# Optimization experiments

Hardware: AMD Instinct MI355X
Metric: run time of the kernel (lower is better)

Reference implementation:

```python
import jax, jax.numpy as jnp
import numpy as np

DIM = 512
HEADS = 8
DIM_HEAD = 64
INNER = HEADS * DIM_HEAD  # 512
HIDDEN = 512 * 4          # mlp_dim * expansion
EPS = 1e-5
SCALE = DIM_HEAD ** -0.5


def layernorm(x, w, b):
    mu = jnp.mean(x, axis=-1, keepdims=True)
    var = jnp.var(x, axis=-1, keepdims=True)
    return (x - mu) * jax.lax.rsqrt(var + EPS) * w + b


def setup_inputs() -> dict:
    key = jax.random.key(0)
    ks = jax.random.split(key, 12)
    B, P, N = 2, 8, 1024  # P must equal HEADS (axis-swap bug in original rearrange)
    s = lambda k, shape, fan: jax.random.normal(k, shape, jnp.float32) * (fan ** -0.5)
    return {
        "x": jax.random.normal(ks[0], (B, P, N, DIM), jnp.float32),
        "ln0_w": jnp.ones((DIM,), jnp.float32),
        "ln0_b": jnp.zeros((DIM,), jnp.float32),
        "ln1_w": jnp.ones((DIM,), jnp.float32),
        "ln1_b": jnp.zeros((DIM,), jnp.float32),
        "w_qkv": s(ks[1], (DIM, 3 * INNER), DIM),
        "w_o": s(ks[2], (INNER, DIM), INNER),
        "b_o": jnp.zeros((DIM,), jnp.float32),
        "w1": s(ks[3], (DIM, HIDDEN), DIM),
        "b1": jnp.zeros((HIDDEN,), jnp.float32),
        "w2": s(ks[4], (HIDDEN, DIM), HIDDEN),
        "b2": jnp.zeros((DIM,), jnp.float32),
    }


def reference(x, ln0_w, ln0_b, ln1_w, ln1_b, w_qkv, w_o, b_o, w1, b1, w2, b2):
    B, P, N, _ = x.shape
    x = layernorm(x, ln0_w, ln0_b)  # outer block norm

    # ---- VisionAttention ----
    h = layernorm(x, ln1_w, ln1_b)
    qkv = h @ w_qkv                                    # [B,P,N,3*INNER]
    q, k, v = jnp.split(qkv, 3, axis=-1)
    def to_heads(t):  # [B,P,N,H*D] -> [B,H,P,N,D]
        return t.reshape(B, P, N, HEADS, DIM_HEAD).transpose(0, 3, 1, 2, 4)
    q, k, v = to_heads(q), to_heads(k), to_heads(v)
    dots = jnp.einsum("bhpnd,bhpmd->bhpnm", q, k) * SCALE  # full NxN scores
    attn = jax.nn.softmax(dots, axis=-1)
    out = jnp.einsum("bhpnm,bhpmd->bhpnd", attn, v)        # [B,H,P,N,D]
    # Faithful to buggy rearrange 'b p h n d -> b p n (h d)': swaps H and P axes.
    out = out.transpose(0, 1, 3, 2, 4).reshape(B, HEADS, N, P * DIM_HEAD)
    out = out @ w_o + b_o                                  # [B,H,N,DIM]
    x = out + x  # residual (valid because P == HEADS)

    # ---- MLP ----
    m = jax.nn.gelu(x @ w1 + b1, approximate=False) @ w2 + b2
    return m + x
```

## Files before the change

### kernel.cpp

```cpp
#include <hip/hip_runtime.h>
#include <hip/hip_bf16.h>
#include <math.h>

#define DIMV 512
#define NTOK 16384
#define NSEQ 1024
#define HEADSV 8
#define PPV 8
#define DHEAD 64
#define QKVW 1536
#define HIDV 2048
#define SC2 0.18033688011112042f

typedef unsigned short ushort;
typedef unsigned int uint;
typedef __attribute__((ext_vector_type(8))) short short8;
typedef __attribute__((ext_vector_type(8))) unsigned short ushort8;
typedef __attribute__((ext_vector_type(4))) unsigned short ushortx4;
typedef __attribute__((ext_vector_type(4))) float floatx4;

__device__ __forceinline__ float bf2f(ushort u){
  union { unsigned int i; float f; } c; c.i = ((unsigned int)u) << 16; return c.f;
}
__device__ __forceinline__ ushort f2bf(float f){
  union { float f; unsigned int i; } c; c.f = f;
  unsigned int u = c.i + 0x7fffu + ((c.i >> 16) & 1u);
  return (ushort)(u >> 16);
}
__device__ __forceinline__ void async_copy16(const void* gptr, void* lptr){
  __builtin_amdgcn_global_load_lds((const __attribute__((address_space(1))) void*)gptr,
                                   (__attribute__((address_space(3))) void*)lptr, 16, 0, 0);
}
__device__ __forceinline__ float fast_gelu(float x){
  float u = x * (2.3022084f + 0.1029435f * x * x);
  return x * __builtin_amdgcn_rcpf(1.f + exp2f(-u));
}

__device__ __forceinline__ void wave_reduce2(float& a, float& b){
  #pragma unroll
  for (int off = 32; off > 0; off >>= 1){
    a += __shfl_down(a, off, 64);
    b += __shfl_down(b, off, 64);
  }
}

__device__ __forceinline__ void wtrans_body(const float* __restrict__ W,
    __hip_bfloat16* __restrict__ Wt, int K, int N, int bx, int by, int t,
    float* tile ){
  int bn = bx * 32, bk = by * 32;
  int tx = t & 31, ty = t >> 5;
  #pragma unroll
  for (int i = 0; i < 32; i += 8)
    tile[(ty + i) * 33 + tx] = W[(size_t)(bk + ty + i) * N + bn + tx];
  __syncthreads();
  #pragma unroll
  for (int i = 0; i < 32; i += 8)
    Wt[(size_t)(bn + ty + i) * K + bk + tx] = __float2bfloat16(tile[tx * 33 + ty + i]);
}

__global__ __launch_bounds__(256) void prep_kernel(const float* __restrict__ x,
    const float* __restrict__ w0, const float* __restrict__ b0,
    const float* __restrict__ w1ln, const float* __restrict__ b1ln,
    __hip_bfloat16* __restrict__ x1, __hip_bfloat16* __restrict__ h,
    const float* __restrict__ wqkv, __hip_bfloat16* __restrict__ wqkvT,
    const float* __restrict__ wo,   __hip_bfloat16* __restrict__ woT,
    const float* __restrict__ w1,   __hip_bfloat16* __restrict__ w1T,
    const float* __restrict__ w2,   __hip_bfloat16* __restrict__ w2T){
  __shared__ float smem[32 * 33];
  int bid = blockIdx.x;
  int t = threadIdx.x;
  if (bid >= NTOK){
    int r = bid - NTOK;
    if (r < 768)        wtrans_body(wqkv, wqkvT, 512, 1536, r % 48, r / 48, t, smem);
    else if (r < 1024){ r -= 768;  wtrans_body(wo, woT, 512, 512,  r % 16, r / 16, t, smem); }
    else if (r < 2048){ r -= 1024; wtrans_body(w1, w1T, 512, 2048, r % 64, r / 64, t, smem); }
    else             { r -= 2048; wtrans_body(w2, w2T, 2048, 512, r % 16, r / 16, t, smem); }
    return;
  }
  float* sm = smem;
  size_t row = bid;
  const float2* xr = (const float2*)(x + row * DIMV);
  float2 v = xr[t];
  float s = v.x + v.y;
  float sq = v.x * v.x + v.y * v.y;
  wave_reduce2(s, sq);
  int wid = t >> 6, lane = t & 63;
  if (lane == 0){ sm[wid] = s; sm[8 + wid] = sq; }
  __syncthreads();
  s  = sm[0] + sm[1] + sm[2] + sm[3];
  sq = sm[8] + sm[9] + sm[10] + sm[11];
  float mu = s * (1.f / DIMV);
  float var = sq * (1.f / DIMV) - mu * mu;
  float r = rsqrtf(var + 1e-5f);
  float2 ww = ((const float2*)w0)[t];
  float2 bb = ((const float2*)b0)[t];
  float2 y;
  y.x = (v.x - mu) * r * ww.x + bb.x;
  y.y = (v.y - mu) * r * ww.y + bb.y;
  ushort2 xb; xb.x = f2bf(y.x); xb.y = f2bf(y.y);
  ((ushort2*)(x1 + row * DIMV))[t] = xb;
  float s2 = y.x + y.y, sq2 = y.x * y.x + y.y * y.y;
  wave_reduce2(s2, sq2);
  __syncthreads();
  if (lane == 0){ sm[wid] = s2; sm[8 + wid] = sq2; }
  __syncthreads();
  s2  = sm[0] + sm[1] + sm[2] + sm[3];
  sq2 = sm[8] + sm[9] + sm[10] + sm[11];
  float mu2 = s2 * (1.f / DIMV);
  float var2 = sq2 * (1.f / DIMV) - mu2 * mu2;
  float r2 = rsqrtf(var2 + 1e-5f);
  float2 w1v = ((const float2*)w1ln)[t];
  float2 b1v = ((const float2*)b1ln)[t];
  float hx = (y.x - mu2) * r2 * w1v.x + b1v.x;
  float hy = (y.y - mu2) * r2 * w1v.y + b1v.y;
  ushort2 hb; hb.x = f2bf(hx); hb.y = f2bf(hy);
  ((ushort2*)(h + row * DIMV))[t] = hb;
}

template<int SWAP>
__global__ __launch_bounds__(512, 2) void gemm_8p(
    const __hip_bfloat16* __restrict__ A,
    const __hip_bfloat16* __restrict__ Bt,
    const float* __restrict__ bias,
    __hip_bfloat16* __restrict__ Cb,
    ushort* __restrict__ vt,
    int M, int N, int K, int gx, int dogelu)
{
  __shared__ __hip_bfloat16 As[2][256 * 64];
  __shared__ __hip_bfloat16 Bs[2][256 * 64];
  int tid = threadIdx.x;
  int l = tid & 63, w = tid >> 6;
  int wr = w >> 2, wc = w & 3;
  int fm = l & 15, quad = l >> 4;

  int bid = blockIdx.x;
  int xcd = bid & 7, idx = bid >> 3;
  int xl = idx % gx, yl = idx / gx;
  size_t bm = (size_t)(xcd * 8 + yl) * 256;
  size_t bn = (size_t)xl * 256;

  int sr = tid >> 3;
  int sc = ((tid & 7) ^ (sr & 7)) * 8;
  const __hip_bfloat16* Ab0 = A + (bm + sr) * (size_t)K + sc;
  const __hip_bfloat16* Bb0 = Bt + (bn + sr) * (size_t)K + sc;
  int ldst = tid * 8;

  int nk = K >> 6;

  #pragma unroll
  for (int j = 0; j < 4; j++)
    async_copy16(Ab0 + (size_t)j * 64 * K, &As[0][j * 4096 + ldst]);
  #pragma unroll
  for (int j = 0; j < 4; j++)
    async_copy16(Bb0 + (size_t)j * 64 * K, &Bs[0][j * 4096 + ldst]);

  floatx4 acc[8][4] = {};

  int arow = wr * 128 + fm;
  int brow = wc * 64 + fm;
  int cx = fm & 7;

  for (int t = 0; t < nk; ++t){
    int cur = t & 1, nxt = cur ^ 1;
    const __hip_bfloat16* Asrc = Ab0 + (size_t)(t + 1) * 64;
    const __hip_bfloat16* Bsrc = Bb0 + (size_t)(t + 1) * 64;
    const __hip_bfloat16* Ac = As[cur];
    const __hip_bfloat16* Bc = Bs[cur];
    short8 bf[4][2], af[2][2];

    if (t + 1 < nk){
      async_copy16(Asrc, &As[nxt][ldst]);
      async_copy16(Asrc + (size_t)64 * K, &As[nxt][4096 + ldst]);
      asm volatile("s_waitcnt vmcnt(2)\n\ts_barrier" ::: "memory");
    } else {
      asm volatile("s_waitcnt vmcnt(0)\n\ts_barrier" ::: "memory");
    }
    #pragma unroll
    for (int ci = 0; ci < 4; ci++)
      #pragma unroll
      for (int kb = 0; kb < 2; kb++)
        bf[ci][kb] = *(const short8*)&Bc[(brow + ci * 16) * 64 + ((kb * 4 + quad) ^ cx) * 8];
    #pragma unroll
    for (int i = 0; i < 2; i++)
      #pragma unroll
      for (int kb = 0; kb < 2; kb++)
        af[i][kb] = *(const short8*)&Ac[(arow + i * 16) * 64 + ((kb * 4 + quad) ^ cx) * 8];
    __builtin_amdgcn_s_setprio(1);
    #pragma unroll
    for (int i = 0; i < 2; i++)
      #pragma unroll
      for (int ci = 0; ci < 4; ci++)
        #pragma unroll
        for (int kb = 0; kb < 2; kb++){
          if (SWAP)
            acc[i][ci] = __builtin_amdgcn_mfma_f32_16x16x32_bf16(bf[ci][kb], af[i][kb], acc[i][ci], 0, 0, 0);
          else
            acc[i][ci] = __builtin_amdgcn_mfma_f32_16x16x32_bf16(af[i][kb], bf[ci][kb], acc[i][ci], 0, 0, 0);
        }
    __builtin_amdgcn_s_setprio(0);
    asm volatile("s_barrier" ::: "memory");

    #pragma unroll
    for (int p = 1; p < 4; p++){
      #pragma unroll
      for (int i = 0; i < 2; i++)
        #pragma unroll
        for (int kb = 0; kb < 2; kb++)
          af[i][kb] = *(const short8*)&Ac[(arow + (p * 2 + i) * 16) * 64 + ((kb * 4 + quad) ^ cx) * 8];
      if (t + 1 < nk){
        if (p == 1){
          async_copy16(Asrc + (size_t)128 * K, &As[nxt][2 * 4096 + ldst]);
          async_copy16(Asrc + (size_t)192 * K, &As[nxt][3 * 4096 + ldst]);
        } else if (p == 2){
          async_copy16(Bsrc, &Bs[nxt][ldst]);
          async_copy16(Bsrc + (size_t)64 * K, &Bs[nxt][4096 + ldst]);
        } else {
          async_copy16(Bsrc + (size_t)128 * K, &Bs[nxt][2 * 4096 + ldst]);
          async_copy16(Bsrc + (size_t)192 * K, &Bs[nxt][3 * 4096 + ldst]);
        }
      }
      asm volatile("s_barrier" ::: "memory");
      __builtin_amdgcn_s_setprio(1);
      #pragma unroll
      for (int i = 0; i < 2; i++)
        #pragma unroll
        for (int ci = 0; ci < 4; ci++)
          #pragma unroll
          for (int kb = 0; kb < 2; kb++){
            if (SWAP)
              acc[p * 2 + i][ci] = __builtin_amdgcn_mfma_f32_16x16x32_bf16(bf[ci][kb], af[i][kb], acc[p * 2 + i][ci], 0, 0, 0);
            else
              acc[p * 2 + i][ci] = __builtin_amdgcn_mfma_f32_16x16x32_bf16(af[i][kb], bf[ci][kb], acc[p * 2 + i][ci], 0, 0, 0);
          }
      __builtin_amdgcn_s_setprio(0);
      asm volatile("s_barrier" ::: "memory");
    }
  }

  if (SWAP){
    #pragma unroll
    for (int ri = 0; ri < 8; ri++){
      size_t row = bm + wr * 128 + ri * 16 + fm;
      size_t rbase = row * (size_t)N + bn + wc * 64 + quad * 4;
      #pragma unroll
      for (int ci = 0; ci < 4; ci++){
        floatx4 v = acc[ri][ci];
        if (bias){
          floatx4 bv = *(const floatx4*)(bias + bn + wc * 64 + ci * 16 + quad * 4);
          #pragma unroll
          for (int r2 = 0; r2 < 4; r2++) v[r2] += bv[r2];
        }
        if (dogelu){
          #pragma unroll
          for (int r2 = 0; r2 < 4; r2++) v[r2] = fast_gelu(v[r2]);
        }
        ushortx4 ob;
        #pragma unroll
        for (int r2 = 0; r2 < 4; r2++) ob[r2] = f2bf(v[r2]);
        *(ushortx4*)((ushort*)Cb + rbase + ci * 16) = ob;
      }
    }
  } else {
    int b = (int)(bm >> 13), p = (int)((bm >> 10) & 7);
    int n0 = (int)(bm & 1023) + wr * 128 + quad * 4;
    #pragma unroll
    for (int ci = 0; ci < 4; ci++){
      int col = (int)bn + wc * 64 + ci * 16 + fm;
      if (col >= 1024){
        int cc = col - 1024, hh = cc >> 6, dd = cc & 63;
        ushort* vdst = vt + ((size_t)((b * 8 + hh) * 8 + p)) * 65536 + (size_t)dd * 1024 + n0;
        #pragma unroll
        for (int ri = 0; ri < 8; ri++){
          ushortx4 v4;
          v4[0] = f2bf(acc[ri][ci][0]); v4[1] = f2bf(acc[ri][ci][1]);
          v4[2] = f2bf(acc[ri][ci][2]); v4[3] = f2bf(acc[ri][ci][3]);
          *(ushortx4*)(vdst + ri * 16) = v4;
        }
      } else {
        float scl = (col < 512) ? SC2 : 1.f;
        #pragma unroll
        for (int ri = 0; ri < 8; ri++){
          size_t rowb = bm + wr * 128 + ri * 16 + quad * 4;
          #pragma unroll
          for (int r2 = 0; r2 < 4; r2++)
            ((ushort*)Cb)[(rowb + r2) * (size_t)N + col] = f2bf(acc[ri][ci][r2] * scl);
        }
      }
    }
  }
}

template<int SWAP>
__global__ __launch_bounds__(256) void gemm_mfma(
    const __hip_bfloat16* __restrict__ A,
    const __hip_bfloat16* __restrict__ Bt,
    const float* __restrict__ bias,
    const __hip_bfloat16* __restrict__ Rb,
    float* __restrict__ Cf,
    __hip_bfloat16* __restrict__ Cb,
    ushort* __restrict__ vt,
    int M, int N, int K, int gx, int dogelu)
{
  __shared__ __hip_bfloat16 As[3][128 * 32];
  __shared__ __hip_bfloat16 Bs[3][128 * 32];
  int tid = threadIdx.x;
  int w = tid >> 6, l = tid & 63;

  int bid = blockIdx.x;
  int xcd = bid & 7, idx = bid >> 3;
  int xl = idx % gx, yl = idx / gx;
  size_t bm = (size_t)(xcd * 16 + yl) * 128;
  size_t bn = (size_t)xl * 128;
  int wm = (w & 1) * 64, wn = (w >> 1) * 64;

  int srow = w * 16 + (l >> 2);
  int gcs = ((l & 3) ^ (srow & 3)) * 8;
  const __hip_bfloat16* Ag0 = A + (bm + srow) * K + gcs;
  const __hip_bfloat16* Ag1 = A + (bm + 64 + srow) * K + gcs;
  const __hip_bfloat16* Bg0 = Bt + (bn + srow) * K + gcs;
  const __hip_bfloat16* Bg1 = Bt + (bn + 64 + srow) * K + gcs;
  int lo = srow * 32 + (l & 3) * 8;

  floatx4 acc[4][4] = {};
  int fm = l & 15;
  int quad = l >> 4;
  int cs = fm & 3;

  int nk = K >> 5;
  async_copy16(Ag0, &As[0][lo]);
  async_copy16(Ag1, &As[0][lo + 64 * 32]);
  async_copy16(Bg0, &Bs[0][lo]);
  async_copy16(Bg1, &Bs[0][lo + 64 * 32]);
  if (nk > 1){
    async_copy16(Ag0 + 32, &As[1][lo]);
    async_copy16(Ag1 + 32, &As[1][lo + 64 * 32]);
    async_copy16(Bg0 + 32, &Bs[1][lo]);
    async_copy16(Bg1 + 32, &Bs[1][lo + 64 * 32]);
  }

  int rb = 0;
  for (int it = 0; it < nk; ++it){
    if (it + 1 < nk)
      asm volatile("s_waitcnt vmcnt(4)\n\ts_barrier" ::: "memory");
    else
      asm volatile("s_waitcnt vmcnt(0)\n\ts_barrier" ::: "memory");
    if (it + 2 < nk){
      int wb = rb >= 1 ? rb - 1 : 2;
      int k0 = (it + 2) << 5;
      async_copy16(Ag0 + k0, &As[wb][lo]);
      async_copy16(Ag1 + k0, &As[wb][lo + 64 * 32]);
      async_copy16(Bg0 + k0, &Bs[wb][lo]);
      async_copy16(Bg1 + k0, &Bs[wb][lo + 64 * 32]);
    }
    const __hip_bfloat16* Ab = As[rb];
    const __hip_bfloat16* Bb = Bs[rb];
    short8 af[4], bf[4];
    #pragma unroll
    for (int i = 0; i < 4; i++){
      af[i] = *(const short8*)&Ab[(wm + i * 16 + fm) * 32 + ((quad ^ cs) * 8)];
      bf[i] = *(const short8*)&Bb[(wn + i * 16 + fm) * 32 + ((quad ^ cs) * 8)];
    }
    #pragma unroll
    for (int mi = 0; mi < 4; mi++)
      #pragma unroll
      for (int ni = 0; ni < 4; ni++){
        if (SWAP)
          acc[mi][ni] = __builtin_amdgcn_mfma_f32_16x16x32_bf16(bf[ni], af[mi], acc[mi][ni], 0, 0, 0);
        else
          acc[mi][ni] = __builtin_amdgcn_mfma_f32_16x16x32_bf16(af[mi], bf[ni], acc[mi][ni], 0, 0, 0);
      }
    rb = rb < 2 ? rb + 1 : 0;
  }

  int rq = quad * 4;
  if (SWAP){
    #pragma unroll
    for (int mi = 0; mi < 4; mi++){
      size_t row = bm + wm + mi * 16 + fm;
      size_t rbase = row * (size_t)N + bn + wn + rq;
      #pragma unroll
      for (int ni = 0; ni < 4; ni++){
        size_t idx2 = rbase + ni * 16;
        floatx4 v = acc[mi][ni];
        if (bias){
          floatx4 bv = *(const floatx4*)(bias + bn + wn + ni * 16 + rq);
          #pragma unroll
          for (int r2 = 0; r2 < 4; r2++) v[r2] += bv[r2];
        }
        if (dogelu){
          #pragma unroll
          for (int r2 = 0; r2 < 4; r2++) v[r2] = fast_gelu(v[r2]);
        }
        if (Rb){
          ushortx4 rbv = *(const ushortx4*)((const ushort*)Rb + idx2);
          #pragma unroll
          for (int r2 = 0; r2 < 4; r2++) v[r2] += bf2f(rbv[r2]);
        }
        if (Cb){
          ushortx4 ob;
          #pragma unroll
          for (int r2 = 0; r2 < 4; r2++) ob[r2] = f2bf(v[r2]);
          *(ushortx4*)((ushort*)Cb + idx2) = ob;
        } else {
          *(floatx4*)(Cf + idx2) = v;
        }
      }
    }
  } else {
    #pragma unroll
    for (int ni = 0; ni < 4; ni++){
      size_t col = bn + wn + ni * 16 + fm;
      float bv = bias ? bias[col] : 0.f;
      #pragma unroll
      for (int mi = 0; mi < 4; mi++){
        #pragma unroll
        for (int r2 = 0; r2 < 4; r2++){
          size_t row = bm + wm + mi * 16 + rq + r2;
          float v = acc[mi][ni][r2] + bv;
          if (dogelu) v = fast_gelu(v);
          size_t idx2 = row * N + col;
          if (Rb) v += bf2f(((const ushort*)Rb)[idx2]);
          Cf[idx2] = v;
        }
      }
    }
  }
}

__global__ __launch_bounds__(256, 4) void attn_mfma(const __hip_bfloat16* __restrict__ qkvp,
                                                    const ushort* __restrict__ vt,
                                                    __hip_bfloat16* __restrict__ outp){
  __shared__ ushort Ks[2][64 * 64];
  __shared__ ushort Vs[2][64 * 64];
  __shared__ ushort Ps[4][32 * 32];
  int tid = threadIdx.x;
  int w = tid >> 6, l = tid & 63;
  int r15 = l & 15, quad = l >> 4, fq = quad * 8;
  int slice = blockIdx.x & 127;
  int qc = blockIdx.x >> 7;
  int b = slice >> 6, hh = (slice >> 3) & 7, p = slice & 7;
  const ushort* base = (const ushort*)qkvp + (size_t)(b * PPV + p) * NSEQ * QKVW;
  const ushort* kb = base + 512 + hh * DHEAD;
  const ushort* vb = vt + (size_t)slice * 65536;

  int s0 = w * 64 + l, s1 = 256 + w * 64 + l;
  int row0 = s0 >> 3, row1 = s1 >> 3;
  int gc0 = (s0 & 7) ^ (row0 & 7), gc1 = (s1 & 7) ^ (row1 & 7);
  const ushort* kp0 = kb + (size_t)row0 * QKVW + gc0 * 8;
  const ushort* kp1 = kb + (size_t)row1 * QKVW + gc1 * 8;
  const ushort* vp0 = vb + (size_t)row0 * 1024 + gc0 * 8;
  const ushort* vp1 = vb + (size_t)row1 * 1024 + gc1 * 8;

  async_copy16(kp0, &Ks[0][s0 * 8]);
  async_copy16(kp1, &Ks[0][s1 * 8]);
  async_copy16(vp0, &Vs[0][s0 * 8]);
  async_copy16(vp1, &Vs[0][s1 * 8]);

  int q0 = qc * 128 + w * 32;
  short8 qf[2][2];
  #pragma unroll
  for (int mi = 0; mi < 2; mi++)
    #pragma unroll
    for (int kk = 0; kk < 2; kk++)
      qf[mi][kk] = *(const short8*)(base + (size_t)(q0 + mi * 16 + r15) * QKVW + hh * DHEAD + kk * 32 + fq);

  floatx4 o[2][4] = {};
  floatx4 lacc[2] = {};
  short8 ones;
  #pragma unroll
  for (int j = 0; j < 8; j++) ones[j] = (short)0x3F80;

  int sw = r15 & 7;
  int swp = (r15 & 3) << 3;
  ushort* PsW = Ps[w];

  for (int it = 0; it < NSEQ / 64; ++it){
    int cur = it & 1;
    asm volatile("s_waitcnt vmcnt(0)\n\ts_barrier" ::: "memory");
    if (it + 1 < NSEQ / 64){
      int nxt = cur ^ 1;
      kp0 += 64 * QKVW; kp1 += 64 * QKVW; vp0 += 64; vp1 += 64;
      async_copy16(kp0, &Ks[nxt][s0 * 8]);
      async_copy16(kp1, &Ks[nxt][s1 * 8]);
      async_copy16(vp0, &Vs[nxt][s0 * 8]);
      async_copy16(vp1, &Vs[nxt][s1 * 8]);
    }
    const ushort* Kb = Ks[cur];
    const ushort* Vb = Vs[cur];

    short8 pf[2][2];
    #pragma unroll
    for (int kk = 0; kk < 2; kk++){
      #pragma unroll
      for (int nn = 0; nn < 2; nn++){
        int ni = kk * 2 + nn;
        int rb2 = (ni * 16 + r15) * 64;
        short8 kf0 = *(const short8*)&Kb[rb2 + (quad ^ sw) * 8];
        short8 kf1 = *(const short8*)&Kb[rb2 + ((4 + quad) ^ sw) * 8];
        floatx4 sA = {}, sB = {};
        sA = __builtin_amdgcn_mfma_f32_16x16x32_bf16(kf0, qf[0][0], sA, 0, 0, 0);
        sA = __builtin_amdgcn_mfma_f32_16x16x32_bf16(kf1, qf[0][1], sA, 0, 0, 0);
        sB = __builtin_amdgcn_mfma_f32_16x16x32_bf16(kf0, qf[1][0], sB, 0, 0, 0);
        sB = __builtin_amdgcn_mfma_f32_16x16x32_bf16(kf1, qf[1][1], sB, 0, 0, 0);
        int wc = (nn * 16 + quad * 4) ^ swp;
        union { float f; uint u; } e0, e1, e2, e3;
        uint2 pk;
        e0.f = exp2f(sA[0]); e1.f = exp2f(sA[1]);
        e2.f = exp2f(sA[2]); e3.f = exp2f(sA[3]);
        pk.x = __builtin_amdgcn_perm(e1.u, e0.u, 0x07060302u);
        pk.y = __builtin_amdgcn_perm(e3.u, e2.u, 0x07060302u);
        *(uint2*)&PsW[r15 * 32 + wc] = pk;
        e0.f = exp2f(sB[0]); e1.f = exp2f(sB[1]);
        e2.f = exp2f(sB[2]); e3.f = exp2f(sB[3]);
        pk.x = __builtin_amdgcn_perm(e1.u, e0.u, 0x07060302u);
        pk.y = __builtin_amdgcn_perm(e3.u, e2.u, 0x07060302u);
        *(uint2*)&PsW[(16 + r15) * 32 + wc] = pk;
      }
      asm volatile("s_waitcnt lgkmcnt(0)" ::: "memory");
      pf[0][kk] = *(const short8*)&PsW[r15 * 32 + (fq ^ swp)];
      pf[1][kk] = *(const short8*)&PsW[(16 + r15) * 32 + (fq ^ swp)];
      asm volatile("s_waitcnt lgkmcnt(0)" ::: "memory");
    }

    #pragma unroll
    for (int mi = 0; mi < 2; mi++)
      #pragma unroll
      for (int kk = 0; kk < 2; kk++)
        lacc[mi] = __builtin_amdgcn_mfma_f32_16x16x32_bf16(ones, pf[mi][kk], lacc[mi], 0, 0, 0);

    #pragma unroll
    for (int dj = 0; dj < 4; dj++){
      int d = dj * 16 + r15;
      short8 vf0 = *(const short8*)&Vb[d * 64 + ((quad) ^ sw) * 8];
      short8 vf1 = *(const short8*)&Vb[d * 64 + ((4 + quad) ^ sw) * 8];
      #pragma unroll
      for (int mi = 0; mi < 2; mi++){
        o[mi][dj] = __builtin_amdgcn_mfma_f32_16x16x32_bf16(vf0, pf[mi][0], o[mi][dj], 0, 0, 0);
        o[mi][dj] = __builtin_amdgcn_mfma_f32_16x16x32_bf16(vf1, pf[mi][1], o[mi][dj], 0, 0, 0);
      }
    }
  }

  #pragma unroll
  for (int mi = 0; mi < 2; mi++){
    float inv = __builtin_amdgcn_rcpf(lacc[mi][0]);
    size_t n = q0 + mi * 16 + r15;
    ushort* orow = (ushort*)outp + ((size_t)((b * HEADSV + hh) * NSEQ + n)) * DIMV + p * DHEAD + quad * 4;
    #pragma unroll
    for (int dj = 0; dj < 4; dj++){
      ushortx4 ov;
      #pragma unroll
      for (int r = 0; r < 4; r++) ov[r] = f2bf(o[mi][dj][r] * inv);
      *(ushortx4*)(orow + dj * 16) = ov;
    }
  }
}

extern "C" void kernel_launch(void* const* d_in, const int* in_sizes, int n_in,
                              void* d_out, int out_size, void* d_ws, size_t ws_size,
                              hipStream_t stream){
  (void)in_sizes; (void)n_in; (void)out_size; (void)ws_size;
  const float* x    = (const float*)d_in[0];
  const float* lw0  = (const float*)d_in[1];
  const float* lb0  = (const float*)d_in[2];
  const float* lw1  = (const float*)d_in[3];
  const float* lb1  = (const float*)d_in[4];
  const float* wqkv = (const float*)d_in[5];
  const float* wo   = (const float*)d_in[6];
  const float* bo   = (const float*)d_in[7];
  const float* w1   = (const float*)d_in[8];
  const float* b1   = (const float*)d_in[9];
  const float* w2   = (const float*)d_in[10];
  const float* b2   = (const float*)d_in[11];
  float* out = (float*)d_out;
  char* ws = (char*)d_ws;
  const size_t MB = 1024 * 1024;

  __hip_bfloat16* x1b  = (__hip_bfloat16*)(ws);
  ushort* vtbuf        = (ushort*)(ws + 32 * MB);
  __hip_bfloat16* x2b  = (__hip_bfloat16*)(ws + 64 * MB);
  __hip_bfloat16* wqkvT= (__hip_bfloat16*)(ws + 80 * MB);
  __hip_bfloat16* woT  = (__hip_bfloat16*)(ws + 82 * MB);
  __hip_bfloat16* w1T  = (__hip_bfloat16*)(ws + 83 * MB);
  __hip_bfloat16* w2T  = (__hip_bfloat16*)(ws + 85 * MB);
  __hip_bfloat16* hB   = (__hip_bfloat16*)(ws + 88 * MB);
  __hip_bfloat16* attnB= hB;
  __hip_bfloat16* qkvB = (__hip_bfloat16*)(ws + 104 * MB);
  __hip_bfloat16* tB   = (__hip_bfloat16*)(ws + 88 * MB);

  prep_kernel<<<NTOK + 3072, 256, 0, stream>>>(
      x, lw0, lb0, lw1, lb1, x1b, hB,
      wqkv, wqkvT, wo, woT, w1, w1T, w2, w2T);

  gemm_8p<0><<<384, 512, 0, stream>>>(
      hB, wqkvT, nullptr, qkvB, vtbuf, NTOK, QKVW, DIMV, 6, 0);

  attn_mfma<<<1024, 256, 0, stream>>>(qkvB, vtbuf, attnB);

  gemm_mfma<1><<<(DIMV / 128) * 128, 256, 0, stream>>>(
      attnB, woT, bo, x1b, nullptr, x2b, nullptr,
      NTOK, DIMV, DIMV, DIMV / 128, 0);

  gemm_8p<1><<<512, 512, 0, stream>>>(
      x2b, w1T, b1, tB, nullptr, NTOK, HIDV, DIMV, 8, 1);

  gemm_mfma<1><<<(DIMV / 128) * 128, 256, 0, stream>>>(
      tB, w2T, b2, x2b, out, nullptr, nullptr,
      NTOK, DIMV, HIDV, DIMV / 128, 0);
}
```

Baseline: 353.9 us.

## Issue all next-tile async loads up front and cut per-phase barriers in GEMM loop

Restructures the double-buffered GEMM main loop. Each iteration now waits for all outstanding loads, then issues every async copy for the next tile at once, instead of spreading them across four compute phases with barriers between them. The s_setprio calls and most s_barriers are removed, leaving one mid-loop barrier. This cuts synchronization overhead and lets compute run uninterrupted, but the full vmcnt(0) wait at the top of each iteration may expose memory latency that the staggered schedule used to hide.

```diff
diff --git a/kernel.cpp b/kernel.cpp
--- a/kernel.cpp
+++ b/kernel.cpp
@@ -162,65 +162,33 @@
 
   for (int t = 0; t < nk; ++t){
     int cur = t & 1, nxt = cur ^ 1;
-    const __hip_bfloat16* Asrc = Ab0 + (size_t)(t + 1) * 64;
-    const __hip_bfloat16* Bsrc = Bb0 + (size_t)(t + 1) * 64;
+    asm volatile("s_waitcnt vmcnt(0)\n\ts_barrier" ::: "memory");
+    if (t + 1 < nk){
+      const __hip_bfloat16* Asrc = Ab0 + (size_t)(t + 1) * 64;
+      const __hip_bfloat16* Bsrc = Bb0 + (size_t)(t + 1) * 64;
+      #pragma unroll
+      for (int j = 0; j < 4; j++)
+        async_copy16(Asrc + (size_t)j * 64 * K, &As[nxt][j * 4096 + ldst]);
+      #pragma unroll
+      for (int j = 0; j < 4; j++)
+        async_copy16(Bsrc + (size_t)j * 64 * K, &Bs[nxt][j * 4096 + ldst]);
+    }
     const __hip_bfloat16* Ac = As[cur];
     const __hip_bfloat16* Bc = Bs[cur];
-    short8 bf[4][2], af[2][2];
-
-    if (t + 1 < nk){
-      async_copy16(Asrc, &As[nxt][ldst]);
-      async_copy16(Asrc + (size_t)64 * K, &As[nxt][4096 + ldst]);
-      asm volatile("s_waitcnt vmcnt(2)\n\ts_barrier" ::: "memory");
-    } else {
-      asm volatile("s_waitcnt vmcnt(0)\n\ts_barrier" ::: "memory");
-    }
+    short8 bf[4][2];
     #pragma unroll
     for (int ci = 0; ci < 4; ci++)
       #pragma unroll
       for (int kb = 0; kb < 2; kb++)
         bf[ci][kb] = *(const short8*)&Bc[(brow + ci * 16) * 64 + ((kb * 4 + quad) ^ cx) * 8];
     #pragma unroll
-    for (int i = 0; i < 2; i++)
-      #pragma unroll
-      for (int kb = 0; kb < 2; kb++)
-        af[i][kb] = *(const short8*)&Ac[(arow + i * 16) * 64 + ((kb * 4 + quad) ^ cx) * 8];
-    __builtin_amdgcn_s_setprio(1);
-    #pragma unroll
-    for (int i = 0; i < 2; i++)
-      #pragma unroll
-      for (int ci = 0; ci < 4; ci++)
-        #pragma unroll
-        for (int kb = 0; kb < 2; kb++){
-          if (SWAP)
-            acc[i][ci] = __builtin_amdgcn_mfma_f32_16x16x32_bf16(bf[ci][kb], af[i][kb], acc[i][ci], 0, 0, 0);
-          else
-            acc[i][ci] = __builtin_amdgcn_mfma_f32_16x16x32_bf16(af[i][kb], bf[ci][kb], acc[i][ci], 0, 0, 0);
-        }
-    __builtin_amdgcn_s_setprio(0);
-    asm volatile("s_barrier" ::: "memory");
-
-    #pragma unroll
-    for (int p = 1; p < 4; p++){
+    for (int p = 0; p < 4; p++){
+      short8 af[2][2];
       #pragma unroll
       for (int i = 0; i < 2; i++)
         #pragma unroll
         for (int kb = 0; kb < 2; kb++)
           af[i][kb] = *(const short8*)&Ac[(arow + (p * 2 + i) * 16) * 64 + ((kb * 4 + quad) ^ cx) * 8];
-      if (t + 1 < nk){
-        if (p == 1){
-          async_copy16(Asrc + (size_t)128 * K, &As[nxt][2 * 4096 + ldst]);
-          async_copy16(Asrc + (size_t)192 * K, &As[nxt][3 * 4096 + ldst]);
-        } else if (p == 2){
-          async_copy16(Bsrc, &Bs[nxt][ldst]);
-          async_copy16(Bsrc + (size_t)64 * K, &Bs[nxt][4096 + ldst]);
-        } else {
-          async_copy16(Bsrc + (size_t)128 * K, &Bs[nxt][2 * 4096 + ldst]);
-          async_copy16(Bsrc + (size_t)192 * K, &Bs[nxt][3 * 4096 + ldst]);
-        }
-      }
-      asm volatile("s_barrier" ::: "memory");
-      __builtin_amdgcn_s_setprio(1);
       #pragma unroll
       for (int i = 0; i < 2; i++)
         #pragma unroll
@@ -232,8 +200,8 @@
             else
               acc[p * 2 + i][ci] = __builtin_amdgcn_mfma_f32_16x16x32_bf16(af[i][kb], bf[ci][kb], acc[p * 2 + i][ci], 0, 0, 0);
           }
-      __builtin_amdgcn_s_setprio(0);
-      asm volatile("s_barrier" ::: "memory");
+      if (p == 1)
+        asm volatile("s_barrier" ::: "memory");
     }
   }
 
```

New measurement: 353.0 us. About the same (-0.3%).
